# Performance work log

Measured on AMD Instinct MI355X. Metric: run time of the kernel, lower is better.

The kernel has to match this reference:

```python
import jax, jax.numpy as jnp
import numpy as np

N = 100000        # nodes
E = 1600000       # edges
IN_NODE = 32
HID = 64
IN_EDGE = 8
OUT = 1


def setup_inputs() -> dict:
    key = jax.random.key(0)
    ks = jax.random.split(key, 16)

    def lin(k, fan_in, fan_out):
        s = 1.0 / np.sqrt(fan_in)
        kw, kb = jax.random.split(k)
        W = jax.random.uniform(kw, (fan_in, fan_out), jnp.float32, -s, s)
        b = jax.random.uniform(kb, (fan_out,), jnp.float32, -s, s)
        return W, b

    x = jax.random.normal(ks[0], (N, IN_NODE), jnp.float32)
    edge_index = jax.random.randint(ks[1], (2, E), 0, N, jnp.int64)
    edge_feat = jax.random.normal(ks[2], (E, IN_EDGE), jnp.float32)

    W0, b0 = lin(ks[3], IN_NODE, HID)        # gcn_in
    W1, b1 = lin(ks[4], HID, HID)            # gcn layer 1
    W2, b2 = lin(ks[5], HID, HID)            # gcn layer 2
    Wm1, bm1 = lin(ks[6], HID * 2 + IN_EDGE, HID)
    Wm2, bm2 = lin(ks[7], HID, HID // 2)
    Wm3, bm3 = lin(ks[8], HID // 2, OUT)

    return {"x": x, "edge_index": edge_index, "edge_feat": edge_feat,
            "W0": W0, "b0": b0, "W1": W1, "b1": b1, "W2": W2, "b2": b2,
            "Wm1": Wm1, "bm1": bm1, "Wm2": Wm2, "bm2": bm2, "Wm3": Wm3, "bm3": bm3}


def _gcn_conv(h, W, b, u, v, dinv):
    # PyG GCNConv: linear transform, symmetric-normalized aggregation with
    # self-loops, then bias. dinv = deg^{-1/2} with deg including self-loop.
    hW = h @ W                                       # [N, F]
    norm = (dinv[u] * dinv[v])[:, None]              # [E, 1]
    agg = jax.ops.segment_sum(hW[u] * norm, v, num_segments=N)
    agg = agg + hW * (dinv * dinv)[:, None]          # self-loop contribution
    return agg + b


def reference(x, edge_index, edge_feat, W0, b0, W1, b1, W2, b2, Wm1, bm1, Wm2, bm2, Wm3, bm3):
    u, v = edge_index[0], edge_index[1]
    # degree of target nodes, including added self-loops
    deg = jax.ops.segment_sum(jnp.ones((E,), x.dtype), v, num_segments=N) + 1.0
    dinv = jax.lax.rsqrt(deg)

    h = jax.nn.relu(_gcn_conv(x, W0, b0, u, v, dinv))
    h = jax.nn.relu(_gcn_conv(h, W1, b1, u, v, dinv))
    h = jax.nn.relu(_gcn_conv(h, W2, b2, u, v, dinv))

    # edge MLP: gather endpoints, concat with edge features
    z = jnp.concatenate([h[u], h[v], edge_feat], axis=-1)   # [E, 2*HID+IN_EDGE]
    z = jax.nn.relu(z @ Wm1 + bm1)
    z = jax.nn.relu(z @ Wm2 + bm2)
    return z @ Wm3 + bm3                                    # [E, OUT]
```

## Files before the change

### kernel.cpp

```cpp
#include <hip/hip_runtime.h>
#include <hip/hip_fp16.h>
#include <cstdint>

#define TPB 256
#define NREP 8
#define SUBCAP 768

typedef _Float16 h2 __attribute__((ext_vector_type(2)));

__device__ __forceinline__ float fdot2(h2 a, h2 b, float c) {
  return __builtin_amdgcn_fdot2(a, b, c, false);
}


__device__ __forceinline__ void fma_row64(float zi, const float* __restrict__ wrow,
                                          float* acc) {
  const float4* w4 = (const float4*)wrow;
#pragma unroll
  for (int j4 = 0; j4 < 16; ++j4) {
    float4 w = w4[j4];
    acc[4 * j4 + 0] = fmaf(zi, w.x, acc[4 * j4 + 0]);
    acc[4 * j4 + 1] = fmaf(zi, w.y, acc[4 * j4 + 1]);
    acc[4 * j4 + 2] = fmaf(zi, w.z, acc[4 * j4 + 2]);
    acc[4 * j4 + 3] = fmaf(zi, w.w, acc[4 * j4 + 3]);
  }
}

__global__ __launch_bounds__(TPB) void prep(int* __restrict__ sub_cnt, int nsub,
                                            int n, const int* __restrict__ ei,
                                            int* __restrict__ flag,
                                            const float* __restrict__ x,
                                            __half* __restrict__ xh) {
  int i = blockIdx.x * TPB + threadIdx.x;
  if (i < nsub) sub_cnt[i] = 0;
  if (i < n) {
    const float4* x4 = (const float4*)(x + (size_t)i * 32);
    __half2* o = (__half2*)(xh + (size_t)i * 32);
#pragma unroll
    for (int j = 0; j < 8; ++j) {
      float4 v = x4[j];
      o[2 * j + 0] = __floats2half2_rn(v.x, v.y);
      o[2 * j + 1] = __floats2half2_rn(v.z, v.w);
    }
  }
  if (i == 0) {
    int o = 0;
    for (int k = 0; k < 32; ++k) o |= ei[2 * k + 1];
    *flag = (o == 0) ? 1 : 0;
  }
}

__global__ __launch_bounds__(TPB) void passA(const int* __restrict__ ei,
                                             const int* __restrict__ flag,
                                             int* __restrict__ sub_cnt,
                                             uint32_t* __restrict__ bkt_buf, int E) {
  int e = blockIdx.x * TPB + threadIdx.x;
  if (e >= E) return;
  int u, v;
  if (*flag) {
    u = ei[2 * (size_t)e];
    v = ei[2 * ((size_t)E + e)];
  } else {
    u = ei[e];
    v = ei[(size_t)E + e];
  }
  int b = v >> 7;
  int sub = b * NREP + (blockIdx.x & (NREP - 1));
  int slot = atomicAdd(&sub_cnt[sub], 1);
  if (slot < SUBCAP)
    bkt_buf[(size_t)sub * SUBCAP + slot] = ((uint32_t)u << 7) | (uint32_t)(v & 127);
}

__global__ void scanB(const int* __restrict__ sub_cnt, int* __restrict__ bkt_base,
                      int* __restrict__ row_ptr, int NBKT, int N,
                      const float* __restrict__ W1e, const float* __restrict__ Wm2,
                      h2* __restrict__ w1p, h2* __restrict__ w2p) {
  __shared__ int tot[1024];
  int t = threadIdx.x;
  int s = 0;
  if (t < NBKT) {
#pragma unroll
    for (int r = 0; r < NREP; ++r) s += min(sub_cnt[t * NREP + r], SUBCAP);
  }
  tot[t] = s;
  __syncthreads();
  for (int off = 1; off < 1024; off <<= 1) {
    int x = (t >= off) ? tot[t - off] : 0;
    __syncthreads();
    tot[t] += x;
    __syncthreads();
  }
  if (t < NBKT) bkt_base[t] = tot[t] - s;
  if (t == 0) row_ptr[N] = tot[NBKT - 1];
  if (t < 256) {
    int j = t >> 2, kk = t & 3;
    w1p[t] =
        h2{(_Float16)W1e[(2 * kk) * 64 + j], (_Float16)W1e[(2 * kk + 1) * 64 + j]};
  }
  if (t < 1024) {
    int j = t >> 5, kk = t & 31;
    w2p[t] =
        h2{(_Float16)Wm2[(2 * kk) * 32 + j], (_Float16)Wm2[(2 * kk + 1) * 32 + j]};
  }
}

__global__ __launch_bounds__(TPB) void passB(const uint32_t* __restrict__ bkt_buf,
                                             const int* __restrict__ sub_cnt,
                                             const int* __restrict__ bkt_base,
                                             int* __restrict__ row_ptr,
                                             float* __restrict__ dinv,
                                             int* __restrict__ u_sorted, int N) {
  int b = blockIdx.x;
  __shared__ int cnt128[128], offs128[128], scnt[NREP];
  int tid = threadIdx.x;
  if (tid < 128) cnt128[tid] = 0;
  if (tid < NREP) scnt[tid] = min(sub_cnt[b * NREP + tid], SUBCAP);
  __syncthreads();
  for (int r = 0; r < NREP; ++r) {
    int m = scnt[r];
    const uint32_t* p = bkt_buf + (size_t)(b * NREP + r) * SUBCAP;
    for (int i = tid; i < m; i += TPB) atomicAdd(&cnt128[p[i] & 127], 1);
  }
  __syncthreads();
  if (tid == 0) {
    int run = 0;
    for (int i = 0; i < 128; ++i) { offs128[i] = run; run += cnt128[i]; }
  }
  __syncthreads();
  int base = bkt_base[b];
  int node = b * 128 + tid;
  if (tid < 128 && node < N) {
    row_ptr[node] = base + offs128[tid];
    dinv[node] = rsqrtf((float)cnt128[tid] + 1.0f);
  }
  if (tid < 128) cnt128[tid] = 0;
  __syncthreads();
  for (int r = 0; r < NREP; ++r) {
    int m = scnt[r];
    const uint32_t* p = bkt_buf + (size_t)(b * NREP + r) * SUBCAP;
    for (int i = tid; i < m; i += TPB) {
      uint32_t pk = p[i];
      int vloc = pk & 127;
      int slot = base + offs128[vloc] + atomicAdd(&cnt128[vloc], 1);
      u_sorted[slot] = (int)(pk >> 7);
    }
  }
}

__global__ __launch_bounds__(TPB) void aggregate32h(const __half* __restrict__ X,
                                                    const int* __restrict__ u_sorted,
                                                    const int* __restrict__ row_ptr,
                                                    const float* __restrict__ dinv,
                                                    float* __restrict__ xagg, int n) {
  int wave = (blockIdx.x * TPB + threadIdx.x) >> 6;
  int lane = threadIdx.x & 63;
  int q = lane >> 4, f2 = lane & 15;
  int node = wave * 4 + q;
  bool valid = node < n;
  int rs = 0, re = 0;
  float dv = 0.f;
  if (valid) { rs = row_ptr[node]; re = row_ptr[node + 1]; dv = dinv[node]; }
  const __half2* selfp = (const __half2*)(X + (size_t)(valid ? node : 0) * 32);
  float2 sf = __half22float2(selfp[f2]);
  float2 acc0 = make_float2(sf.x * dv, sf.y * dv);
  float2 acc1 = make_float2(0.f, 0.f);
  int sb = q << 4;
  for (int base = rs; base < re; base += 16) {
    int m = re - base;
    if (m > 16) m = 16;
    int uj = 0;
    float wj = 0.f;
    if (f2 < m) { uj = u_sorted[base + f2]; wj = dinv[uj]; }
    int k = 0;
    for (; k + 1 < m; k += 2) {
      int u0 = __shfl(uj, sb + k), u1 = __shfl(uj, sb + k + 1);
      float w0 = __shfl(wj, sb + k), w1 = __shfl(wj, sb + k + 1);
      float2 v0 = __half22float2(((const __half2*)(X + (size_t)u0 * 32))[f2]);
      float2 v1 = __half22float2(((const __half2*)(X + (size_t)u1 * 32))[f2]);
      acc0.x = fmaf(v0.x, w0, acc0.x);
      acc0.y = fmaf(v0.y, w0, acc0.y);
      acc1.x = fmaf(v1.x, w1, acc1.x);
      acc1.y = fmaf(v1.y, w1, acc1.y);
    }
    if (k < m) {
      int u0 = __shfl(uj, sb + k);
      float w0 = __shfl(wj, sb + k);
      float2 v0 = __half22float2(((const __half2*)(X + (size_t)u0 * 32))[f2]);
      acc0.x = fmaf(v0.x, w0, acc0.x);
      acc0.y = fmaf(v0.y, w0, acc0.y);
    }
  }
  if (valid) {
    float2 r = make_float2(dv * (acc0.x + acc1.x), dv * (acc0.y + acc1.y));
    ((float2*)(xagg + (size_t)node * 32))[f2] = r;
  }
}

__global__ __launch_bounds__(TPB) void lin32_br(const float* __restrict__ A,
                                                const float* __restrict__ W,
                                                const float* __restrict__ bias,
                                                float* __restrict__ B, int n) {
  __shared__ __align__(16) float Ws[32 * 64];
  __shared__ float bs[64];
  int tid = threadIdx.x;
  for (int i = tid; i < 32 * 64; i += TPB) Ws[i] = W[i];
  if (tid < 64) bs[tid] = bias[tid];
  __syncthreads();
  int node = blockIdx.x * TPB + tid;
  if (node >= n) return;
  const float4* a4 = (const float4*)(A + (size_t)node * 32);
  float acc[64];
#pragma unroll
  for (int j = 0; j < 64; ++j) acc[j] = bs[j];
  for (int i4 = 0; i4 < 8; ++i4) {
    float4 z = a4[i4];
    fma_row64(z.x, &Ws[(4 * i4 + 0) * 64], acc);
    fma_row64(z.y, &Ws[(4 * i4 + 1) * 64], acc);
    fma_row64(z.z, &Ws[(4 * i4 + 2) * 64], acc);
    fma_row64(z.w, &Ws[(4 * i4 + 3) * 64], acc);
  }
  float4* b4 = (float4*)(B + (size_t)node * 64);
#pragma unroll
  for (int j4 = 0; j4 < 16; ++j4)
    b4[j4] = make_float4(fmaxf(acc[4 * j4 + 0], 0.f), fmaxf(acc[4 * j4 + 1], 0.f),
                         fmaxf(acc[4 * j4 + 2], 0.f), fmaxf(acc[4 * j4 + 3], 0.f));
}

__global__ __launch_bounds__(TPB) void lin_node64h(const float* __restrict__ A,
                                                   const float* __restrict__ W,
                                                   __half* __restrict__ Bh, int n) {
  __shared__ __align__(16) float Ws[64 * 64];
  int tid = threadIdx.x;
  for (int i = tid; i < 64 * 64; i += TPB) Ws[i] = W[i];
  __syncthreads();
  int node = blockIdx.x * TPB + tid;
  if (node >= n) return;
  const float4* a4 = (const float4*)(A + (size_t)node * 64);
  float acc[64];
#pragma unroll
  for (int j = 0; j < 64; ++j) acc[j] = 0.f;
  for (int i4 = 0; i4 < 16; ++i4) {
    float4 z = a4[i4];
    fma_row64(z.x, &Ws[(4 * i4 + 0) * 64], acc);
    fma_row64(z.y, &Ws[(4 * i4 + 1) * 64], acc);
    fma_row64(z.z, &Ws[(4 * i4 + 2) * 64], acc);
    fma_row64(z.w, &Ws[(4 * i4 + 3) * 64], acc);
  }
  __half2* o2 = (__half2*)(Bh + (size_t)node * 64);
#pragma unroll
  for (int j2 = 0; j2 < 32; ++j2)
    o2[j2] = __floats2half2_rn(acc[2 * j2 + 0], acc[2 * j2 + 1]);
}

__global__ __launch_bounds__(TPB) void aggregateh(const __half* __restrict__ Bh,
                                                  const int* __restrict__ u_sorted,
                                                  const int* __restrict__ row_ptr,
                                                  const float* __restrict__ dinv,
                                                  const float* __restrict__ bias,
                                                  float* __restrict__ A, int n) {
  int wave = (blockIdx.x * TPB + threadIdx.x) >> 6;
  int lane = threadIdx.x & 63;
  int half = lane >> 5, f2 = lane & 31;
  int node = wave * 2 + half;
  bool valid = node < n;
  int rs = 0, re = 0;
  float dv = 0.f;
  if (valid) { rs = row_ptr[node]; re = row_ptr[node + 1]; dv = dinv[node]; }
  const __half2* selfp = (const __half2*)(Bh + (size_t)(valid ? node : 0) * 64);
  float2 sf = __half22float2(selfp[f2]);
  float2 acc0 = make_float2(sf.x * dv, sf.y * dv);
  float2 acc1 = make_float2(0.f, 0.f);
  float2 acc2 = make_float2(0.f, 0.f);
  float2 acc3 = make_float2(0.f, 0.f);
  int sb = half << 5;
  for (int base = rs; base < re; base += 32) {
    int m = re - base;
    if (m > 32) m = 32;
    int uj = 0;
    float wj = 0.f;
    if (f2 < m) { uj = u_sorted[base + f2]; wj = dinv[uj]; }
    int k = 0;
    for (; k + 3 < m; k += 4) {
      int u0 = __shfl(uj, sb + k), u1 = __shfl(uj, sb + k + 1);
      int u2 = __shfl(uj, sb + k + 2), u3 = __shfl(uj, sb + k + 3);
      float w0 = __shfl(wj, sb + k), w1 = __shfl(wj, sb + k + 1);
      float w2 = __shfl(wj, sb + k + 2), w3 = __shfl(wj, sb + k + 3);
      float2 v0 = __half22float2(((const __half2*)(Bh + (size_t)u0 * 64))[f2]);
      float2 v1 = __half22float2(((const __half2*)(Bh + (size_t)u1 * 64))[f2]);
      float2 v2 = __half22float2(((const __half2*)(Bh + (size_t)u2 * 64))[f2]);
      float2 v3 = __half22float2(((const __half2*)(Bh + (size_t)u3 * 64))[f2]);
      acc0.x = fmaf(v0.x, w0, acc0.x); acc0.y = fmaf(v0.y, w0, acc0.y);
      acc1.x = fmaf(v1.x, w1, acc1.x); acc1.y = fmaf(v1.y, w1, acc1.y);
      acc2.x = fmaf(v2.x, w2, acc2.x); acc2.y = fmaf(v2.y, w2, acc2.y);
      acc3.x = fmaf(v3.x, w3, acc3.x); acc3.y = fmaf(v3.y, w3, acc3.y);
    }
    for (; k < m; ++k) {
      int u0 = __shfl(uj, sb + k);
      float w0 = __shfl(wj, sb + k);
      float2 v0 = __half22float2(((const __half2*)(Bh + (size_t)u0 * 64))[f2]);
      acc0.x = fmaf(v0.x, w0, acc0.x);
      acc0.y = fmaf(v0.y, w0, acc0.y);
    }
  }
  if (valid) {
    float2 bi = ((const float2*)bias)[f2];
    float2 r;
    r.x = fmaxf(dv * ((acc0.x + acc1.x) + (acc2.x + acc3.x)) + bi.x, 0.f);
    r.y = fmaxf(dv * ((acc0.y + acc1.y) + (acc2.y + acc3.y)) + bi.y, 0.f);
    ((float2*)(A + (size_t)node * 64))[f2] = r;
  }
}

__global__ __launch_bounds__(TPB) void lin_ab(const float* __restrict__ A,
                                              const float* __restrict__ W,
                                              __half* __restrict__ apre,
                                              __half* __restrict__ bpre, int n) {
  __shared__ __align__(16) float Ws[128 * 64];
  int tid = threadIdx.x;
  for (int i = tid; i < 128 * 64; i += TPB) Ws[i] = W[i];
  __syncthreads();
  int node = blockIdx.x * TPB + tid;
  if (node >= n) return;
  const float4* a4 = (const float4*)(A + (size_t)node * 64);
  float acc[64];
#pragma unroll
  for (int j = 0; j < 64; ++j) acc[j] = 0.f;
  for (int i4 = 0; i4 < 16; ++i4) {
    float4 z = a4[i4];
    fma_row64(z.x, &Ws[(4 * i4 + 0) * 64], acc);
    fma_row64(z.y, &Ws[(4 * i4 + 1) * 64], acc);
    fma_row64(z.z, &Ws[(4 * i4 + 2) * 64], acc);
    fma_row64(z.w, &Ws[(4 * i4 + 3) * 64], acc);
  }
  __half2* o2 = (__half2*)(apre + (size_t)node * 64);
#pragma unroll
  for (int j2 = 0; j2 < 32; ++j2)
    o2[j2] = __floats2half2_rn(acc[2 * j2 + 0], acc[2 * j2 + 1]);
#pragma unroll
  for (int j = 0; j < 64; ++j) acc[j] = 0.f;
  for (int i4 = 0; i4 < 16; ++i4) {
    float4 z = a4[i4];
    fma_row64(z.x, &Ws[(64 + 4 * i4 + 0) * 64], acc);
    fma_row64(z.y, &Ws[(64 + 4 * i4 + 1) * 64], acc);
    fma_row64(z.z, &Ws[(64 + 4 * i4 + 2) * 64], acc);
    fma_row64(z.w, &Ws[(64 + 4 * i4 + 3) * 64], acc);
  }
  o2 = (__half2*)(bpre + (size_t)node * 64);
#pragma unroll
  for (int j2 = 0; j2 < 32; ++j2)
    o2[j2] = __floats2half2_rn(acc[2 * j2 + 0], acc[2 * j2 + 1]);
}

__global__ __launch_bounds__(TPB) void edge_mlp(
    const __half* __restrict__ apre, const __half* __restrict__ bpre,
    const int* __restrict__ ei, const int* __restrict__ flag,
    const float* __restrict__ EF, const h2* __restrict__ w1p,
    const float* __restrict__ bm1, const h2* __restrict__ w2p,
    const float* __restrict__ bm2, const float* __restrict__ Wm3,
    const float* __restrict__ bm3, float* __restrict__ out, int E) {
  int e = blockIdx.x * TPB + threadIdx.x;
  if (e >= E) return;
  int u, v;
  if (*flag) {
    u = ei[2 * (size_t)e];
    v = ei[2 * ((size_t)E + e)];
  } else {
    u = ei[e];
    v = ei[(size_t)E + e];
  }
  const h2* a2 = (const h2*)(apre + (size_t)u * 64);
  const h2* b2 = (const h2*)(bpre + (size_t)v * 64);
  const float4* ef4 = (const float4*)(EF + (size_t)e * 8);
  float4 z0 = ef4[0], z1 = ef4[1];
  h2 efh[4];
  efh[0] = h2{(_Float16)z0.x, (_Float16)z0.y};
  efh[1] = h2{(_Float16)z0.z, (_Float16)z0.w};
  efh[2] = h2{(_Float16)z1.x, (_Float16)z1.y};
  efh[3] = h2{(_Float16)z1.z, (_Float16)z1.w};
  const h2 selLo = h2{(_Float16)1.f, (_Float16)0.f};
  const h2 selHi = h2{(_Float16)0.f, (_Float16)1.f};

  float acc[64];
#pragma unroll
  for (int j = 0; j < 64; ++j) {
    h2 sel = (j & 1) ? selHi : selLo;
    float a = fdot2(a2[j >> 1], sel, bm1[j]);
    a = fdot2(b2[j >> 1], sel, a);
    const h2* wp = w1p + j * 4;
    a = fdot2(efh[0], wp[0], a);
    a = fdot2(efh[1], wp[1], a);
    a = fdot2(efh[2], wp[2], a);
    a = fdot2(efh[3], wp[3], a);
    acc[j] = a;
  }

  h2 zh[32];
#pragma unroll
  for (int i2 = 0; i2 < 32; ++i2)
    zh[i2] = h2{(_Float16)fmaxf(acc[2 * i2 + 0], 0.f),
                (_Float16)fmaxf(acc[2 * i2 + 1], 0.f)};

  float o = bm3[0];
#pragma unroll
  for (int j = 0; j < 32; ++j) {
    float z = bm2[j];
    const h2* wp = w2p + j * 32;
#pragma unroll
    for (int kk = 0; kk < 32; ++kk) z = fdot2(zh[kk], wp[kk], z);
    o = fmaf(fmaxf(z, 0.f), Wm3[j], o);
  }
  out[e] = o;
}

extern "C" void kernel_launch(void* const* d_in, const int* in_sizes, int n_in,
                              void* d_out, int out_size, void* d_ws, size_t ws_size,
                              hipStream_t stream) {
  const float* x   = (const float*)d_in[0];
  const int*   ei  = (const int*)d_in[1];
  const float* ef  = (const float*)d_in[2];
  const float* W0  = (const float*)d_in[3];
  const float* b0  = (const float*)d_in[4];
  const float* W1  = (const float*)d_in[5];
  const float* b1  = (const float*)d_in[6];
  const float* W2  = (const float*)d_in[7];
  const float* b2  = (const float*)d_in[8];
  const float* Wm1 = (const float*)d_in[9];
  const float* bm1 = (const float*)d_in[10];
  const float* Wm2 = (const float*)d_in[11];
  const float* bm2 = (const float*)d_in[12];
  const float* Wm3 = (const float*)d_in[13];
  const float* bm3 = (const float*)d_in[14];
  float* out = (float*)d_out;

  const int N = in_sizes[0] / 32;
  const int E = in_sizes[2] / 8;
  const int NBKT = (N + 127) >> 7;
  const int nsub = NBKT * NREP;

  char* p = (char*)d_ws;
  auto carve = [&](size_t bytes) {
    void* r = (void*)p;
    p += ((bytes + 255) / 256) * 256;
    return r;
  };
  int*      row_ptr  = (int*)carve((size_t)(N + 1) * 4);
  float*    dinv     = (float*)carve((size_t)N * 4);
  int*      flag     = (int*)carve(256);
  h2*       w1p      = (h2*)carve(256 * 4);
  h2*       w2p      = (h2*)carve(1024 * 4);
  int*      sub_cnt  = (int*)carve((size_t)nsub * 4);
  int*      bkt_base = (int*)carve((size_t)(NBKT + 1) * 4);
  uint32_t* bkt_buf  = (uint32_t*)carve((size_t)nsub * SUBCAP * 4);
  int*      u_sorted = (int*)carve((size_t)E * 4);
  float*    hA       = (float*)carve((size_t)N * 64 * 4);
  float*    hB       = (float*)carve((size_t)N * 64 * 4);
  __half*   linh     = (__half*)carve((size_t)N * 64 * 2);
  __half*   apreh    = (__half*)carve((size_t)N * 64 * 2);
  __half*   bpreh    = (__half*)carve((size_t)N * 64 * 2);
  if ((size_t)(p - (char*)d_ws) > ws_size) return;

  float* xagg = hB;
  __half* xh = apreh;

  const int EB = (E + TPB - 1) / TPB;
  const int NB = (N + TPB - 1) / TPB;
  const int AB2 = (((N + 1) / 2) + 3) / 4;
  const int AB4 = (((N + 3) / 4) + 3) / 4;

  prep<<<NB, TPB, 0, stream>>>(sub_cnt, nsub, N, ei, flag, x, xh);
  passA<<<EB, TPB, 0, stream>>>(ei, flag, sub_cnt, bkt_buf, E);
  scanB<<<1, 1024, 0, stream>>>(sub_cnt, bkt_base, row_ptr, NBKT, N,
                                Wm1 + 128 * 64, Wm2, w1p, w2p);
  passB<<<NBKT, TPB, 0, stream>>>(bkt_buf, sub_cnt, bkt_base, row_ptr, dinv,
                                  u_sorted, N);

  aggregate32h<<<AB4, TPB, 0, stream>>>(xh, u_sorted, row_ptr, dinv, xagg, N);
  lin32_br<<<NB, TPB, 0, stream>>>(xagg, W0, b0, hA, N);
  lin_node64h<<<NB, TPB, 0, stream>>>(hA, W1, linh, N);
  aggregateh<<<AB2, TPB, 0, stream>>>(linh, u_sorted, row_ptr, dinv, b1, hB, N);
  lin_node64h<<<NB, TPB, 0, stream>>>(hB, W2, linh, N);
  aggregateh<<<AB2, TPB, 0, stream>>>(linh, u_sorted, row_ptr, dinv, b2, hA, N);

  lin_ab<<<NB, TPB, 0, stream>>>(hA, Wm1, apreh, bpreh, N);

  edge_mlp<<<EB, TPB, 0, stream>>>(apreh, bpreh, ei, flag, ef, w1p, bm1, w2p, bm2,
                                   Wm3, bm3, out, E);
}
```

Baseline: 473.8 us.

## Block-local bucket staging in passA and fuse first two node linears

passA now handles an 8192-edge chunk per block. Each block counts and prefix-sums bucket sizes in shared memory, stages the packed edges, then reserves space with one global atomic per bucket and copies the edges out in contiguous runs. This replaces one global atomic per edge spread over 8 sub-buckets. The first GCN linear (32->64, relu) is also fused with the second layer's 64->64 transform, so the fp32 hA intermediate is never written or read back. Risks: the serial per-thread copy loop in passA, reading edge indices twice, and heavy register use in the fused kernel.

New measurement: 400.7 us. 15.4% less time.

```diff
diff --git a/kernel.cpp b/kernel.cpp
--- a/kernel.cpp
+++ b/kernel.cpp
@@ -3,8 +3,8 @@
 #include <cstdint>
 
 #define TPB 256
-#define NREP 8
-#define SUBCAP 768
+#define CHUNK 8192
+#define BKTCAP 4096
 
 typedef _Float16 h2 __attribute__((ext_vector_type(2)));
 
@@ -26,13 +26,13 @@
   }
 }
 
-__global__ __launch_bounds__(TPB) void prep(int* __restrict__ sub_cnt, int nsub,
+__global__ __launch_bounds__(TPB) void prep(int* __restrict__ gcnt, int nbkt,
                                             int n, const int* __restrict__ ei,
                                             int* __restrict__ flag,
                                             const float* __restrict__ x,
                                             __half* __restrict__ xh) {
   int i = blockIdx.x * TPB + threadIdx.x;
-  if (i < nsub) sub_cnt[i] = 0;
+  if (i < nbkt) gcnt[i] = 0;
   if (i < n) {
     const float4* x4 = (const float4*)(x + (size_t)i * 32);
     __half2* o = (__half2*)(xh + (size_t)i * 32);
@@ -52,36 +52,75 @@
 
 __global__ __launch_bounds__(TPB) void passA(const int* __restrict__ ei,
                                              const int* __restrict__ flag,
-                                             int* __restrict__ sub_cnt,
-                                             uint32_t* __restrict__ bkt_buf, int E) {
-  int e = blockIdx.x * TPB + threadIdx.x;
-  if (e >= E) return;
-  int u, v;
-  if (*flag) {
-    u = ei[2 * (size_t)e];
-    v = ei[2 * ((size_t)E + e)];
-  } else {
-    u = ei[e];
-    v = ei[(size_t)E + e];
-  }
-  int b = v >> 7;
-  int sub = b * NREP + (blockIdx.x & (NREP - 1));
-  int slot = atomicAdd(&sub_cnt[sub], 1);
-  if (slot < SUBCAP)
-    bkt_buf[(size_t)sub * SUBCAP + slot] = ((uint32_t)u << 7) | (uint32_t)(v & 127);
-}
-
-__global__ void scanB(const int* __restrict__ sub_cnt, int* __restrict__ bkt_base,
+                                             int* __restrict__ gcnt,
+                                             uint32_t* __restrict__ bkt_buf,
+                                             int E, int NBKT) {
+  __shared__ int base0[1024], cur[1024], s4[TPB];
+  __shared__ uint32_t stage[CHUNK];
+  int tid = threadIdx.x;
+  int start = blockIdx.x * CHUNK;
+  int nloc = E - start;
+  if (nloc > CHUNK) nloc = CHUNK;
+  for (int i = tid; i < NBKT; i += TPB) cur[i] = 0;
+  __syncthreads();
+  bool f64 = (*flag != 0);
+  for (int i = tid; i < nloc; i += TPB) {
+    int e = start + i;
+    int v = f64 ? ei[2 * ((size_t)E + e)] : ei[(size_t)E + e];
+    atomicAdd(&cur[v >> 7], 1);
+  }
+  __syncthreads();
+  int b0i = 4 * tid;
+  int c0 = (b0i + 0 < NBKT) ? cur[b0i + 0] : 0;
+  int c1 = (b0i + 1 < NBKT) ? cur[b0i + 1] : 0;
+  int c2 = (b0i + 2 < NBKT) ? cur[b0i + 2] : 0;
+  int c3 = (b0i + 3 < NBKT) ? cur[b0i + 3] : 0;
+  int s = c0 + c1 + c2 + c3;
+  s4[tid] = s;
+  __syncthreads();
+  for (int off = 1; off < TPB; off <<= 1) {
+    int xv = (tid >= off) ? s4[tid - off] : 0;
+    __syncthreads();
+    s4[tid] += xv;
+    __syncthreads();
+  }
+  int excl = s4[tid] - s;
+  if (b0i + 0 < NBKT) base0[b0i + 0] = excl;
+  if (b0i + 1 < NBKT) base0[b0i + 1] = excl + c0;
+  if (b0i + 2 < NBKT) base0[b0i + 2] = excl + c0 + c1;
+  if (b0i + 3 < NBKT) base0[b0i + 3] = excl + c0 + c1 + c2;
+  __syncthreads();
+  for (int i = tid; i < NBKT; i += TPB) cur[i] = base0[i];
+  __syncthreads();
+  for (int i = tid; i < nloc; i += TPB) {
+    int e = start + i;
+    int u, v;
+    if (f64) { u = ei[2 * (size_t)e]; v = ei[2 * ((size_t)E + e)]; }
+    else     { u = ei[e];             v = ei[(size_t)E + e]; }
+    int b = v >> 7;
+    int slot = atomicAdd(&cur[b], 1);
+    stage[slot] = ((uint32_t)u << 7) | (uint32_t)(v & 127);
+  }
+  __syncthreads();
+  for (int b = tid; b < NBKT; b += TPB) {
+    int s0 = base0[b];
+    int c = cur[b] - s0;
+    if (c > 0) {
+      int g = atomicAdd(&gcnt[b], c);
+      int cc = min(c, max(0, BKTCAP - g));
+      uint32_t* dst = bkt_buf + (size_t)b * BKTCAP + g;
+      for (int i = 0; i < cc; ++i) dst[i] = stage[s0 + i];
+    }
+  }
+}
+
+__global__ void scanB(const int* __restrict__ gcnt, int* __restrict__ bkt_base,
                       int* __restrict__ row_ptr, int NBKT, int N,
                       const float* __restrict__ W1e, const float* __restrict__ Wm2,
                       h2* __restrict__ w1p, h2* __restrict__ w2p) {
   __shared__ int tot[1024];
   int t = threadIdx.x;
-  int s = 0;
-  if (t < NBKT) {
-#pragma unroll
-    for (int r = 0; r < NREP; ++r) s += min(sub_cnt[t * NREP + r], SUBCAP);
-  }
+  int s = (t < NBKT) ? min(gcnt[t], BKTCAP) : 0;
   tot[t] = s;
   __syncthreads();
   for (int off = 1; off < 1024; off <<= 1) {
@@ -91,7 +130,7 @@
     __syncthreads();
   }
   if (t < NBKT) bkt_base[t] = tot[t] - s;
-  if (t == 0) row_ptr[N] = tot[NBKT - 1];
+  if (t == 0) row_ptr[N] = tot[1023];
   if (t < 256) {
     int j = t >> 2, kk = t & 3;
     w1p[t] =
@@ -105,22 +144,19 @@
 }
 
 __global__ __launch_bounds__(TPB) void passB(const uint32_t* __restrict__ bkt_buf,
-                                             const int* __restrict__ sub_cnt,
+                                             const int* __restrict__ gcnt,
                                              const int* __restrict__ bkt_base,
                                              int* __restrict__ row_ptr,
                                              float* __restrict__ dinv,
                                              int* __restrict__ u_sorted, int N) {
   int b = blockIdx.x;
-  __shared__ int cnt128[128], offs128[128], scnt[NREP];
+  __shared__ int cnt128[128], offs128[128];
   int tid = threadIdx.x;
   if (tid < 128) cnt128[tid] = 0;
-  if (tid < NREP) scnt[tid] = min(sub_cnt[b * NREP + tid], SUBCAP);
-  __syncthreads();
-  for (int r = 0; r < NREP; ++r) {
-    int m = scnt[r];
-    const uint32_t* p = bkt_buf + (size_t)(b * NREP + r) * SUBCAP;
-    for (int i = tid; i < m; i += TPB) atomicAdd(&cnt128[p[i] & 127], 1);
-  }
+  __syncthreads();
+  int m = min(gcnt[b], BKTCAP);
+  const uint32_t* p = bkt_buf + (size_t)b * BKTCAP;
+  for (int i = tid; i < m; i += TPB) atomicAdd(&cnt128[p[i] & 127], 1);
   __syncthreads();
   if (tid == 0) {
     int run = 0;
@@ -135,15 +171,11 @@
   }
   if (tid < 128) cnt128[tid] = 0;
   __syncthreads();
-  for (int r = 0; r < NREP; ++r) {
-    int m = scnt[r];
-    const uint32_t* p = bkt_buf + (size_t)(b * NREP + r) * SUBCAP;
-    for (int i = tid; i < m; i += TPB) {
-      uint32_t pk = p[i];
-      int vloc = pk & 127;
-      int slot = base + offs128[vloc] + atomicAdd(&cnt128[vloc], 1);
-      u_sorted[slot] = (int)(pk >> 7);
-    }
+  for (int i = tid; i < m; i += TPB) {
+    uint32_t pk = p[i];
+    int vloc = pk & 127;
+    int slot = base + offs128[vloc] + atomicAdd(&cnt128[vloc], 1);
+    u_sorted[slot] = (int)(pk >> 7);
   }
 }
 
@@ -196,34 +228,56 @@
   }
 }
 
-__global__ __launch_bounds__(TPB) void lin32_br(const float* __restrict__ A,
-                                                const float* __restrict__ W,
-                                                const float* __restrict__ bias,
-                                                float* __restrict__ B, int n) {
-  __shared__ __align__(16) float Ws[32 * 64];
+__global__ __launch_bounds__(TPB) void lin32_64(const float* __restrict__ A,
+                                                const float* __restrict__ W0,
+                                                const float* __restrict__ b0v,
+                                                const float* __restrict__ W1,
+                                                __half* __restrict__ Bh, int n) {
+  __shared__ __align__(16) float W0s[32 * 64];
+  __shared__ __align__(16) float W1s[64 * 64];
   __shared__ float bs[64];
   int tid = threadIdx.x;
-  for (int i = tid; i < 32 * 64; i += TPB) Ws[i] = W[i];
-  if (tid < 64) bs[tid] = bias[tid];
+  for (int i = tid; i < 32 * 64; i += TPB) W0s[i] = W0[i];
+  for (int i = tid; i < 64 * 64; i += TPB) W1s[i] = W1[i];
+  if (tid < 64) bs[tid] = b0v[tid];
   __syncthreads();
   int node = blockIdx.x * TPB + tid;
   if (node >= n) return;
   const float4* a4 = (const float4*)(A + (size_t)node * 32);
-  float acc[64];
-#pragma unroll
-  for (int j = 0; j < 64; ++j) acc[j] = bs[j];
+  float h1[64];
+#pragma unroll
+  for (int j = 0; j < 64; ++j) h1[j] = bs[j];
   for (int i4 = 0; i4 < 8; ++i4) {
     float4 z = a4[i4];
-    fma_row64(z.x, &Ws[(4 * i4 + 0) * 64], acc);
-    fma_row64(z.y, &Ws[(4 * i4 + 1) * 64], acc);
-    fma_row64(z.z, &Ws[(4 * i4 + 2) * 64], acc);
-    fma_row64(z.w, &Ws[(4 * i4 + 3) * 64], acc);
-  }
-  float4* b4 = (float4*)(B + (size_t)node * 64);
-#pragma unroll
-  for (int j4 = 0; j4 < 16; ++j4)
-    b4[j4] = make_float4(fmaxf(acc[4 * j4 + 0], 0.f), fmaxf(acc[4 * j4 + 1], 0.f),
-                         fmaxf(acc[4 * j4 + 2], 0.f), fmaxf(acc[4 * j4 + 3], 0.f));
+    fma_row64(z.x, &W0s[(4 * i4 + 0) * 64], h1);
+    fma_row64(z.y, &W0s[(4 * i4 + 1) * 64], h1);
+    fma_row64(z.z, &W0s[(4 * i4 + 2) * 64], h1);
+    fma_row64(z.w, &W0s[(4 * i4 + 3) * 64], h1);
+  }
+#pragma unroll
+  for (int j = 0; j < 64; ++j) h1[j] = fmaxf(h1[j], 0.f);
+  __half2* o2 = (__half2*)(Bh + (size_t)node * 64);
+#pragma unroll
+  for (int hf = 0; hf < 2; ++hf) {
+    float acc[32];
+#pragma unroll
+    for (int j = 0; j < 32; ++j) acc[j] = 0.f;
+    for (int i = 0; i < 64; ++i) {
+      float zi = h1[i];
+      const float4* w4 = (const float4*)&W1s[i * 64 + hf * 32];
+#pragma unroll
+      for (int j4 = 0; j4 < 8; ++j4) {
+        float4 w = w4[j4];
+        acc[4 * j4 + 0] = fmaf(zi, w.x, acc[4 * j4 + 0]);
+        acc[4 * j4 + 1] = fmaf(zi, w.y, acc[4 * j4 + 1]);
+        acc[4 * j4 + 2] = fmaf(zi, w.z, acc[4 * j4 + 2]);
+        acc[4 * j4 + 3] = fmaf(zi, w.w, acc[4 * j4 + 3]);
+      }
+    }
+#pragma unroll
+    for (int j2 = 0; j2 < 16; ++j2)
+      o2[hf * 16 + j2] = __floats2half2_rn(acc[2 * j2 + 0], acc[2 * j2 + 1]);
+  }
 }
 
 __global__ __launch_bounds__(TPB) void lin_node64h(const float* __restrict__ A,
@@ -435,7 +489,6 @@
   const int N = in_sizes[0] / 32;
   const int E = in_sizes[2] / 8;
   const int NBKT = (N + 127) >> 7;
-  const int nsub = NBKT * NREP;
 
   char* p = (char*)d_ws;
   auto carve = [&](size_t bytes) {
@@ -448,9 +501,9 @@
   int*      flag     = (int*)carve(256);
   h2*       w1p      = (h2*)carve(256 * 4);
   h2*       w2p      = (h2*)carve(1024 * 4);
-  int*      sub_cnt  = (int*)carve((size_t)nsub * 4);
+  int*      gcnt     = (int*)carve((size_t)NBKT * 4);
   int*      bkt_base = (int*)carve((size_t)(NBKT + 1) * 4);
-  uint32_t* bkt_buf  = (uint32_t*)carve((size_t)nsub * SUBCAP * 4);
+  uint32_t* bkt_buf  = (uint32_t*)carve((size_t)NBKT * BKTCAP * 4);
   int*      u_sorted = (int*)carve((size_t)E * 4);
   float*    hA       = (float*)carve((size_t)N * 64 * 4);
   float*    hB       = (float*)carve((size_t)N * 64 * 4);
@@ -464,19 +517,19 @@
 
   const int EB = (E + TPB - 1) / TPB;
   const int NB = (N + TPB - 1) / TPB;
+  const int EBC = (E + CHUNK - 1) / CHUNK;
   const int AB2 = (((N + 1) / 2) + 3) / 4;
   const int AB4 = (((N + 3) / 4) + 3) / 4;
 
-  prep<<<NB, TPB, 0, stream>>>(sub_cnt, nsub, N, ei, flag, x, xh);
-  passA<<<EB, TPB, 0, stream>>>(ei, flag, sub_cnt, bkt_buf, E);
-  scanB<<<1, 1024, 0, stream>>>(sub_cnt, bkt_base, row_ptr, NBKT, N,
+  prep<<<NB, TPB, 0, stream>>>(gcnt, NBKT, N, ei, flag, x, xh);
+  passA<<<EBC, TPB, 0, stream>>>(ei, flag, gcnt, bkt_buf, E, NBKT);
+  scanB<<<1, 1024, 0, stream>>>(gcnt, bkt_base, row_ptr, NBKT, N,
                                 Wm1 + 128 * 64, Wm2, w1p, w2p);
-  passB<<<NBKT, TPB, 0, stream>>>(bkt_buf, sub_cnt, bkt_base, row_ptr, dinv,
+  passB<<<NBKT, TPB, 0, stream>>>(bkt_buf, gcnt, bkt_base, row_ptr, dinv,
                                   u_sorted, N);
 
   aggregate32h<<<AB4, TPB, 0, stream>>>(xh, u_sorted, row_ptr, dinv, xagg, N);
-  lin32_br<<<NB, TPB, 0, stream>>>(xagg, W0, b0, hA, N);
-  lin_node64h<<<NB, TPB, 0, stream>>>(hA, W1, linh, N);
+  lin32_64<<<NB, TPB, 0, stream>>>(xagg, W0, b0, W1, linh, N);
   aggregateh<<<AB2, TPB, 0, stream>>>(linh, u_sorted, row_ptr, dinv, b1, hB, N);
   lin_node64h<<<NB, TPB, 0, stream>>>(hB, W2, linh, N);
   aggregateh<<<AB2, TPB, 0, stream>>>(linh, u_sorted, row_ptr, dinv, b2, hA, N);
```
